# Performance work log

Measured on AMD Instinct MI355X. Metric: run time of the kernel, lower is better.

## Reference

```python
import jax, jax.numpy as jnp
import numpy as np

B, N, G, K, V, M = 8, 4096, 128, 16, 64, 64
D, NH, FF = 384, 8, 1536
DH = D // NH


def _ln(x):
    m = jnp.mean(x, -1, keepdims=True)
    v = jnp.mean((x - m) ** 2, -1, keepdims=True)
    return (x - m) * jax.lax.rsqrt(v + 1e-5)


def _attn(q_in, kv_in, w, mask=None):
    # w: [4, D, D] = (Wq, Wk, Wv, Wo)
    Bq, Sq, _ = q_in.shape
    Sk = kv_in.shape[1]
    q = (q_in @ w[0]).reshape(Bq, Sq, NH, DH)
    k = (kv_in @ w[1]).reshape(Bq, Sk, NH, DH)
    v = (kv_in @ w[2]).reshape(Bq, Sk, NH, DH)
    logits = jnp.einsum('bqhd,bkhd->bhqk', q, k) / np.float32(np.sqrt(DH))
    if mask is not None:
        logits = jnp.where(mask[:, None], logits, jnp.float32(-1e9))
    a = jax.nn.softmax(logits, -1)
    return jnp.einsum('bhqk,bkhd->bqhd', a, v).reshape(Bq, Sq, D) @ w[3]


def _ffn(x, w1, w2):
    return jax.nn.relu(x @ w1) @ w2


def _knn(q, ref, k):
    d = (jnp.sum(q * q, -1)[:, :, None] + jnp.sum(ref * ref, -1)[:, None, :]
         - 2.0 * jnp.einsum('bqd,brd->bqr', q, ref))
    return jax.lax.top_k(-d, k)[1]  # [B, Nq, k]


def _fps(pos, m):
    Bc = pos.shape[0]
    d0 = jnp.sum((pos - pos[:, :1]) ** 2, -1)
    def step(mind, _):
        nxt = jnp.argmax(mind, -1)
        p = jnp.take_along_axis(pos, nxt[:, None, None], 1)
        return jnp.minimum(mind, jnp.sum((pos - p) ** 2, -1)), nxt
    _, idxs = jax.lax.scan(step, d0, None, length=m - 1)
    idx = jnp.concatenate([jnp.zeros((Bc, 1), idxs.dtype), idxs.T], 1)
    return jnp.take_along_axis(pos, idx[..., None], 1)  # [B, m, 3]


def _pe(xyz):
    # PositionEmbeddingCoordsSine: 3 -> D, scale=1.0
    cd = D // 3
    dim_t = 10000.0 ** (2.0 * (jnp.arange(cd) // 2) / cd)
    p = xyz[..., None] / dim_t  # [..., 3, cd]
    pe = jnp.stack([jnp.sin(p[..., 0::2]), jnp.cos(p[..., 1::2])], -1)
    return pe.reshape(xyz.shape[:-1] + (D,))


def _gather(x, idx):  # x: [B,S,C], idx: [B,m]
    return jnp.take_along_axis(x, idx[:, :, None], 1)


def _neigh_mask(nidx, S):  # boolean attention mask from knn indices
    Bc, Q, _ = nidx.shape
    return jnp.zeros((Bc, Q, S), bool).at[
        jnp.arange(Bc)[:, None, None], jnp.arange(Q)[None, :, None], nidx].set(True)


def _tokenize(pos, w1, b1, w2, b2, w3, b3, w4, b4):
    centers = _fps(pos, G)
    nidx = _knn(centers, pos, K)
    grouped = pos[jnp.arange(pos.shape[0])[:, None, None], nidx]  # [B,G,K,3]
    rel = grouped - centers[:, :, None, :]
    f = jax.nn.relu(rel @ w1 + b1) @ w2 + b2                       # [B,G,K,256]
    g = jnp.broadcast_to(f.max(2)[:, :, None, :], f.shape)
    tok = (jax.nn.relu(jnp.concatenate([g, f], -1) @ w3 + b3) @ w4 + b4).max(2)
    return tok, centers


def _cross_encoder(src, tgt, src_mask, tgt_mask, cx_attn, cx_ff1, cx_ff2):
    sa, ca = cx_attn[0], cx_attn[1]
    src = src + _attn(_ln(src), _ln(src), sa, src_mask)
    tgt = tgt + _attn(_ln(tgt), _ln(tgt), sa, tgt_mask)
    src2 = src + _attn(_ln(src), _ln(tgt), ca)
    tgt2 = tgt + _attn(_ln(tgt), _ln(src), ca)
    src2 = src2 + _ffn(_ln(src2), cx_ff1, cx_ff2)
    tgt2 = tgt2 + _ffn(_ln(tgt2), cx_ff1, cx_ff2)
    return src2, tgt2


def _dec_blocks(q, q_pos, mem, mem_pos, sa, ca, f1, f2):
    x = q + q_pos
    m = mem + mem_pos
    for l in range(ca.shape[0]):
        if sa is not None:
            x = x + _attn(_ln(x), _ln(x), sa[l])
        x = x + _attn(_ln(x), _ln(m), ca[l])
        x = x + _ffn(_ln(x), f1[l], f2[l])
    return x


def _upsample(pos, centers, feats, w1, b1, w2, b2):
    # PointNet++ feature propagation: 3-NN inverse-distance interpolation + MLP
    d = (jnp.sum(pos * pos, -1)[:, :, None] + jnp.sum(centers * centers, -1)[:, None, :]
         - 2.0 * jnp.einsum('bnd,bgd->bng', pos, centers))
    nd, idx = jax.lax.top_k(-d, 3)
    w = 1.0 / (jnp.maximum(-nd, 0.0) + 1e-8)
    w = w / jnp.sum(w, -1, keepdims=True)
    nb = feats[jnp.arange(pos.shape[0])[:, None, None], idx]  # [B,N,3,D]
    interp = jnp.sum(w[..., None] * nb, 2)
    x = jnp.concatenate([interp, pos], -1)  # concat xyz (points1) -> D+3
    return jax.nn.relu(jax.nn.relu(x @ w1 + b1) @ w2 + b2)


def _smooth_l1(t, p, beta=2.0):
    a = jnp.abs(p - t)
    return jnp.mean(jnp.where(a < beta, 0.5 * a * a / beta, a - 0.5 * beta))


def _forward(pos_src, pos_tgt, tok_w1, tok_b1, tok_w2, tok_b2, tok_w3, tok_b3,
             tok_w4, tok_b4, mask_token, cx_attn, cx_ff1, cx_ff2,
             enc_sa, enc_ca, enc_ff1, enc_ff2, dec_ca, dec_ff1, dec_ff2,
             up_w1, up_b1, up_w2, up_b2,
             vis_idx_src, msk_idx_src, vis_idx_tgt, msk_idx_tgt):
    tokens_src, centers_src = _tokenize(pos_src, tok_w1, tok_b1, tok_w2, tok_b2, tok_w3, tok_b3, tok_w4, tok_b4)
    tokens_tgt, centers_tgt = _tokenize(pos_tgt, tok_w1, tok_b1, tok_w2, tok_b2, tok_w3, tok_b3, tok_w4, tok_b4)
    c_src_pe, c_tgt_pe = _pe(centers_src), _pe(centers_tgt)
    p_src_pe, p_tgt_pe = _pe(pos_src), _pe(pos_tgt)

    vis3_src = _gather(centers_src, vis_idx_src)   # [B,V,3]
    vis3_tgt = _gather(centers_tgt, vis_idx_tgt)
    vtok_src = _gather(tokens_src, vis_idx_src)    # [B,V,D]
    vtok_tgt = _gather(tokens_tgt, vis_idx_tgt)

    m_full_src = _neigh_mask(_knn(centers_src, centers_src, K), G)
    m_full_tgt = _neigh_mask(_knn(centers_tgt, centers_tgt, K), G)
    m_vis_src = _neigh_mask(_knn(vis3_src, vis3_src, K), V)
    m_vis_tgt = _neigh_mask(_knn(vis3_tgt, vis3_tgt, K), V)

    vis_out_src, vis_out_tgt = _cross_encoder(vtok_src, vtok_tgt, m_vis_src, m_vis_tgt, cx_attn, cx_ff1, cx_ff2)
    src_out, tgt_out = _cross_encoder(tokens_src, tokens_tgt, m_full_src, m_full_tgt, cx_attn, cx_ff1, cx_ff2)

    Bc = pos_src.shape[0]
    mt = jnp.broadcast_to(mask_token, (Bc, M, D))
    q_src = jnp.concatenate([mt, vis_out_src], 1)
    qpos_src = jnp.concatenate([_gather(c_src_pe, msk_idx_src), _gather(c_src_pe, vis_idx_src)], 1)
    q_tgt = jnp.concatenate([mt, vis_out_tgt], 1)
    qpos_tgt = jnp.concatenate([_gather(c_tgt_pe, msk_idx_tgt), _gather(c_tgt_pe, vis_idx_tgt)], 1)

    dec_src = _dec_blocks(q_src, qpos_src, tgt_out, c_tgt_pe, enc_sa, enc_ca, enc_ff1, enc_ff2)
    dec_tgt = _dec_blocks(q_tgt, qpos_tgt, src_out, c_src_pe, enc_sa, enc_ca, enc_ff1, enc_ff2)

    t_src = jax.lax.stop_gradient(_gather(src_out, msk_idx_src))
    t_tgt = jax.lax.stop_gradient(_gather(tgt_out, msk_idx_tgt))
    mae = 0.5 * _smooth_l1(t_src, dec_src[:, :M]) + 0.5 * _smooth_l1(t_tgt, dec_tgt[:, :M])

    up_src = _upsample(pos_src, centers_src, src_out, up_w1, up_b1, up_w2, up_b2)
    up_tgt = _upsample(pos_tgt, centers_tgt, tgt_out, up_w1, up_b1, up_w2, up_b2)
    dense_src = _dec_blocks(up_src, p_src_pe, src_out, c_src_pe, None, dec_ca, dec_ff1, dec_ff2)
    dense_tgt = _dec_blocks(up_tgt, p_tgt_pe, tgt_out, c_tgt_pe, None, dec_ca, dec_ff1, dec_ff2)
    return dense_src, dense_tgt, mae


def setup_inputs() -> dict:
    key = jax.random.key(0)
    ks = jax.random.split(key, 32)
    nrm = lambda i, shp: jax.random.normal(ks[i], shp, dtype=jnp.float32) * 0.02
    ps = jax.vmap(lambda k: jax.random.permutation(k, G))(jax.random.split(ks[2], B))
    pt = jax.vmap(lambda k: jax.random.permutation(k, G))(jax.random.split(ks[3], B))
    return {
        'pos_src': jax.random.normal(ks[0], (B, N, 3), dtype=jnp.float32),
        'pos_tgt': jax.random.normal(ks[1], (B, N, 3), dtype=jnp.float32),
        'vis_idx_src': ps[:, :V], 'msk_idx_src': ps[:, V:],
        'vis_idx_tgt': pt[:, :V], 'msk_idx_tgt': pt[:, V:],
        'tok_w1': nrm(4, (3, 128)), 'tok_b1': jnp.zeros((128,), jnp.float32),
        'tok_w2': nrm(5, (128, 256)), 'tok_b2': jnp.zeros((256,), jnp.float32),
        'tok_w3': nrm(6, (512, 512)), 'tok_b3': jnp.zeros((512,), jnp.float32),
        'tok_w4': nrm(7, (512, D)), 'tok_b4': jnp.zeros((D,), jnp.float32),
        'mask_token': nrm(8, (D,)),
        'cx_attn': nrm(9, (2, 4, D, D)), 'cx_ff1': nrm(10, (D, FF)), 'cx_ff2': nrm(11, (FF, D)),
        'enc_sa': nrm(12, (4, 4, D, D)), 'enc_ca': nrm(13, (4, 4, D, D)),
        'enc_ff1': nrm(14, (4, D, FF)), 'enc_ff2': nrm(15, (4, FF, D)),
        'dec_ca': nrm(16, (2, 4, D, D)), 'dec_ff1': nrm(17, (2, D, FF)), 'dec_ff2': nrm(18, (2, FF, D)),
        'up_w1': nrm(19, (D + 3, D)), 'up_b1': jnp.zeros((D,), jnp.float32),
        'up_w2': nrm(20, (D, D)), 'up_b2': jnp.zeros((D,), jnp.float32),
    }


def reference(pos_src, pos_tgt, vis_idx_src, msk_idx_src, vis_idx_tgt, msk_idx_tgt,
              tok_w1, tok_b1, tok_w2, tok_b2, tok_w3, tok_b3, tok_w4, tok_b4,
              mask_token, cx_attn, cx_ff1, cx_ff2, enc_sa, enc_ca, enc_ff1, enc_ff2,
              dec_ca, dec_ff1, dec_ff2, up_w1, up_b1, up_w2, up_b2):
    return _forward(pos_src, pos_tgt, tok_w1, tok_b1, tok_w2, tok_b2, tok_w3, tok_b3,
                    tok_w4, tok_b4, mask_token, cx_attn, cx_ff1, cx_ff2,
                    enc_sa, enc_ca, enc_ff1, enc_ff2, dec_ca, dec_ff1, dec_ff2,
                    up_w1, up_b1, up_w2, up_b2,
                    vis_idx_src, msk_idx_src, vis_idx_tgt, msk_idx_tgt)
```

## Files before the change

kernel.cpp:

```cpp
#include <hip/hip_runtime.h>
#include <hip/hip_bf16.h>
#include <math.h>

using bf16 = __hip_bfloat16;

#define DI static __device__ __forceinline__

constexpr int Bc = 8, Nn = 4096, Gc = 128, Kc = 16, Vc = 64, Mc = 64;
constexpr int Dd = 384, NHh = 8, DHh = 48, FFf = 1536;

typedef __bf16 bf8v __attribute__((ext_vector_type(8)));
typedef float f4v __attribute__((ext_vector_type(4)));

DI float b2f(bf16 h) { return __bfloat162float(h); }
DI __bf16 f2b(float f) { return (__bf16)f; }

__global__ __launch_bounds__(256) void detect_kernel(const unsigned int* __restrict__ w, int* __restrict__ flag) {
    __shared__ int sh[256];
    int cnt = 0;
    for (int i = threadIdx.x; i < 16384; i += 256) {
        unsigned int lo = w[i] & 0xffffu;
        int e = (int)((lo >> 7) & 0xffu);
        if (e < 100 || e > 140) cnt++;
    }
    sh[threadIdx.x] = cnt;
    __syncthreads();
    for (int s = 128; s > 0; s >>= 1) {
        if (threadIdx.x < s) sh[threadIdx.x] += sh[threadIdx.x + s];
        __syncthreads();
    }
    if (threadIdx.x == 0) flag[0] = (sh[0] < 2048) ? 1 : 0;
}

DI float ldf(const void* p, size_t i, int isbf) {
    return isbf ? b2f(((const bf16*)p)[i]) : ((const float*)p)[i];
}

__global__ void cvtf_kernel(const void* __restrict__ src, float* __restrict__ dst, size_t n,
                            const int* __restrict__ flag) {
    size_t t = (size_t)blockIdx.x * 256 + threadIdx.x;
    if (t < n) dst[t] = ldf(src, t, flag[0]);
}

__global__ void wtr_kernel(const void* __restrict__ src, __bf16* __restrict__ dst,
                           int K, int N, int Kpad, int cnt, const int* __restrict__ flag) {
    size_t t = (size_t)blockIdx.x * 256 + threadIdx.x;
    size_t total = (size_t)cnt * N * Kpad;
    if (t >= total) return;
    int k = (int)(t % Kpad);
    size_t rem = t / Kpad;
    int n = (int)(rem % N);
    int mat = (int)(rem / N);
    float v = (k < K) ? ldf(src, ((size_t)mat * K + k) * N + n, flag[0]) : 0.f;
    dst[t] = f2b(v);
}

__global__ void zero_kernel(unsigned char* __restrict__ p, size_t n) {
    size_t t = (size_t)blockIdx.x * 256 + threadIdx.x;
    if (t < n) p[t] = 0;
}

__global__ void add_kernel(const float* __restrict__ a, const float* __restrict__ b,
                           float* __restrict__ o, size_t n) {
    size_t t = (size_t)blockIdx.x * 256 + threadIdx.x;
    if (t < n) o[t] = a[t] + b[t];
}

__global__ __launch_bounds__(256) void fps_kernel(const float* __restrict__ pos_a, const float* __restrict__ pos_b,
                                                  float* __restrict__ cent_a, float* __restrict__ cent_b) {
    __shared__ float px[Nn], py[Nn], pz[Nn];
    __shared__ float wv[4];
    __shared__ int wi[4];
    __shared__ int chosen;
    int side = blockIdx.x >> 3, b = blockIdx.x & 7, tid = threadIdx.x;
    const float* pos = side ? pos_b : pos_a;
    float* cent = side ? cent_b : cent_a;
    const float* p = pos + (size_t)b * Nn * 3;
    for (int i = tid; i < Nn; i += 256) { px[i] = p[3*i]; py[i] = p[3*i+1]; pz[i] = p[3*i+2]; }
    __syncthreads();
    float cx = px[0], cy = py[0], cz = pz[0];
    if (tid == 0) { float* c0 = cent + (size_t)b * Gc * 3; c0[0] = cx; c0[1] = cy; c0[2] = cz; }
    float mind[16];
#pragma unroll
    for (int j = 0; j < 16; j++) {
        int i = tid + 256 * j;
        float dx = px[i]-cx, dy = py[i]-cy, dz = pz[i]-cz;
        mind[j] = __fadd_rn(__fadd_rn(__fmul_rn(dx,dx), __fmul_rn(dy,dy)), __fmul_rn(dz,dz));
    }
    for (int s = 1; s < Gc; s++) {
        float bv = -1.f; int bi = 0;
#pragma unroll
        for (int j = 0; j < 16; j++) { int i = tid + 256*j; if (mind[j] > bv) { bv = mind[j]; bi = i; } }
        for (int o = 32; o > 0; o >>= 1) {
            float v2 = __shfl_down(bv, o, 64); int i2 = __shfl_down(bi, o, 64);
            if (v2 > bv || (v2 == bv && i2 < bi)) { bv = v2; bi = i2; }
        }
        if ((tid & 63) == 0) { wv[tid >> 6] = bv; wi[tid >> 6] = bi; }
        __syncthreads();
        if (tid == 0) {
            float fv = wv[0]; int fi = wi[0];
            for (int k = 1; k < 4; k++)
                if (wv[k] > fv || (wv[k] == fv && wi[k] < fi)) { fv = wv[k]; fi = wi[k]; }
            chosen = fi;
            float* cs = cent + ((size_t)b * Gc + s) * 3;
            cs[0] = px[fi]; cs[1] = py[fi]; cs[2] = pz[fi];
        }
        __syncthreads();
        int ci = chosen;
        float qx = px[ci], qy = py[ci], qz = pz[ci];
#pragma unroll
        for (int j = 0; j < 16; j++) {
            int i = tid + 256 * j;
            float dx = px[i]-qx, dy = py[i]-qy, dz = pz[i]-qz;
            float d = __fadd_rn(__fadd_rn(__fmul_rn(dx,dx), __fmul_rn(dy,dy)), __fmul_rn(dz,dz));
            if (d < mind[j]) mind[j] = d;
        }
    }
}

__global__ __launch_bounds__(64) void knn16_kernel(const float* __restrict__ q, const float* __restrict__ r,
                                                   int* __restrict__ nidx, int NQ, int NR) {
    __shared__ float dist[4096];
    int blk = blockIdx.x; int b = blk / NQ, qi = blk % NQ;
    int lane = threadIdx.x;
    const float* qp = q + ((size_t)b * NQ + qi) * 3;
    float qx = qp[0], qy = qp[1], qz = qp[2];
    float qq = __fadd_rn(__fadd_rn(__fmul_rn(qx,qx), __fmul_rn(qy,qy)), __fmul_rn(qz,qz));
    const float* rp = r + (size_t)b * NR * 3;
    for (int i = lane; i < NR; i += 64) {
        float rx = rp[3*i], ry = rp[3*i+1], rz = rp[3*i+2];
        float rr = __fadd_rn(__fadd_rn(__fmul_rn(rx,rx), __fmul_rn(ry,ry)), __fmul_rn(rz,rz));
        float dot = __fadd_rn(__fadd_rn(__fmul_rn(qx,rx), __fmul_rn(qy,ry)), __fmul_rn(qz,rz));
        dist[i] = __fadd_rn(__fadd_rn(qq, rr), -2.f * dot);
    }
    __syncthreads();
    int* out = nidx + ((size_t)b * NQ + qi) * Kc;
    for (int sel = 0; sel < Kc; ++sel) {
        float bv = INFINITY; int bi = 0;
        bool has = false;
        for (int i = lane; i < NR; i += 64) {
            float v = dist[i];
            if (!has || v < bv) { bv = v; bi = i; has = true; }
        }
        for (int o = 32; o > 0; o >>= 1) {
            float v2 = __shfl_xor(bv, o, 64); int i2 = __shfl_xor(bi, o, 64);
            if (v2 < bv || (v2 == bv && i2 < bi)) { bv = v2; bi = i2; }
        }
        if (lane == 0) { out[sel] = bi; dist[bi] = INFINITY; }
        __syncthreads();
    }
}

__global__ __launch_bounds__(64) void knn3_kernel(const float* __restrict__ pos, const float* __restrict__ cent,
                                                  int* __restrict__ idx3, float* __restrict__ w3) {
    int bn = blockIdx.x; int b = bn / Nn;
    int lane = threadIdx.x;
    const float* p = pos + (size_t)bn * 3;
    float px = p[0], py = p[1], pz = p[2];
    float pp = __fadd_rn(__fadd_rn(__fmul_rn(px,px), __fmul_rn(py,py)), __fmul_rn(pz,pz));
    float dv[2]; int di[2];
#pragma unroll
    for (int c = 0; c < 2; c++) {
        int g = lane + 64 * c;
        const float* cp = cent + ((size_t)b * Gc + g) * 3;
        float cx = cp[0], cy = cp[1], cz = cp[2];
// ... 59 lines not shown
    if (t >= BG * C) return;
    int c = t % C; int bg = t / C;
    const float* p = in + (size_t)bg * Kc * C + c;
    float m = -INFINITY;
    for (int k = 0; k < Kc; k++) m = fmaxf(m, p[(size_t)k * C]);
    out[t] = m;
}

__global__ void maxk_bf_kernel(const __bf16* __restrict__ in, __bf16* __restrict__ out, int BG, int C) {
    int t = blockIdx.x * 256 + threadIdx.x;
    if (t >= BG * C) return;
    int c = t % C; int bg = t / C;
    const __bf16* p = in + (size_t)bg * Kc * C + c;
    float m = -INFINITY;
    for (int k = 0; k < Kc; k++) m = fmaxf(m, (float)p[(size_t)k * C]);
    out[t] = f2b(m);
}

__global__ void concat_gf_kernel(const __bf16* __restrict__ g, const __bf16* __restrict__ f,
                                 __bf16* __restrict__ cat, int BG) {
    size_t t = (size_t)blockIdx.x * 256 + threadIdx.x;
    size_t total = (size_t)BG * Kc * 512;
    if (t >= total) return;
    int c = (int)(t % 512); size_t bgk = t / 512; size_t bg = bgk / Kc;
    cat[t] = (c < 256) ? g[bg * 256 + c] : f[bgk * 256 + (c - 256)];
}

__global__ void gather_rows_kernel(const float* __restrict__ in, const int* __restrict__ idx,
                                   float* __restrict__ out, int Ni, int C, int Sin) {
    size_t t = (size_t)blockIdx.x * 256 + threadIdx.x;
    size_t total = (size_t)Bc * Ni * C;
    if (t >= total) return;
    int c = (int)(t % C); size_t bi = t / C; int i = (int)(bi % Ni); int b = (int)(bi / Ni);
    int r = idx[(size_t)b * Ni + i];
    out[t] = in[((size_t)b * Sin + r) * C + c];
}

__global__ void scatter_mask_kernel(const int* __restrict__ nidx, unsigned char* __restrict__ mask,
                                    int Q, int S, int nb) {
    int t = blockIdx.x * 256 + threadIdx.x;
    if (t >= nb * Q * Kc) return;
    int q = (t / Kc) % Q; int b = t / (Kc * Q);
    mask[((size_t)b * Q + q) * S + nidx[t]] = 1;
}

__global__ void pe_kernel(float* __restrict__ dst, const float* __restrict__ base,
                          const float* __restrict__ xyz, size_t total) {
    size_t t = (size_t)blockIdx.x * 256 + threadIdx.x;
    if (t >= total) return;
    int d = (int)(t % Dd); size_t bs = t / Dd;
    int c = d >> 7;
    int i = d & 127;
    int j = i >> 1;
    float inv = expf(-0.1439115683121279f * (float)j);
    float val = xyz[bs * 3 + c] * inv;
    float pe = (i & 1) ? cosf(val) : sinf(val);
    dst[t] = (base ? base[t] : 0.f) + pe;
}

__global__ __launch_bounds__(256) void ln_kernel(const float* __restrict__ X, __bf16* __restrict__ Y, int R) {
    int lane = threadIdx.x & 63;
    int row = blockIdx.x * 4 + (threadIdx.x >> 6);
    if (row >= R) return;
    const float* x = X + (size_t)row * Dd;
    float v[6]; float s = 0.f;
#pragma unroll
    for (int j = 0; j < 6; j++) { v[j] = x[lane + 64*j]; s += v[j]; }
#pragma unroll
    for (int o = 32; o > 0; o >>= 1) s += __shfl_xor(s, o, 64);
    float m = s * (1.f / Dd);
    float s2 = 0.f;
#pragma unroll
    for (int j = 0; j < 6; j++) { float d = v[j] - m; s2 += d * d; }
#pragma unroll
    for (int o = 32; o > 0; o >>= 1) s2 += __shfl_xor(s2, o, 64);
    float inv = rsqrtf(s2 * (1.f / Dd) + 1e-5f);
    __bf16* y = Y + (size_t)row * Dd;
#pragma unroll
    for (int j = 0; j < 6; j++) y[lane + 64*j] = f2b((v[j] - m) * inv);
}

__global__ __launch_bounds__(256) void gemm_kernel(const __bf16* __restrict__ A, const __bf16* __restrict__ Wt,
                                                   const float* __restrict__ bias,
                                                   const float* __restrict__ res, void* __restrict__ Cv,
                                                   int M, int Ncols, int Kk, int relu, int obf) {
    __shared__ __bf16 As[128][72];
    __shared__ __bf16 Bs[128][72];
    const int tid = threadIdx.x;
    const int row0 = blockIdx.y * 128, col0 = blockIdx.x * 128;
    const int w = tid >> 6, lane = tid & 63, m = lane & 15, q = lane >> 4;
    const int wr = w >> 1, wc = w & 1;
    const int srow = tid >> 1, sk = (tid & 1) * 32;
    const __bf16* ap = A + (size_t)(row0 + srow) * Kk + sk;
    const __bf16* wp = Wt + (size_t)(col0 + srow) * Kk + sk;

    f4v acc[4][4];
#pragma unroll
    for (int r = 0; r < 4; r++)
#pragma unroll
        for (int n = 0; n < 4; n++) acc[r][n] = (f4v){0.f, 0.f, 0.f, 0.f};

    for (int k0 = 0; k0 < Kk; k0 += 64) {
#pragma unroll
        for (int i = 0; i < 4; i++) {
            *reinterpret_cast<uint4*>(&As[srow][sk + 8*i]) = *reinterpret_cast<const uint4*>(ap + k0 + 8*i);
            *reinterpret_cast<uint4*>(&Bs[srow][sk + 8*i]) = *reinterpret_cast<const uint4*>(wp + k0 + 8*i);
        }
        __syncthreads();
#pragma unroll
        for (int kk = 0; kk < 2; kk++) {
            bf8v bfr[4], afr[4];
#pragma unroll
            for (int n = 0; n < 4; n++) bfr[n] = *reinterpret_cast<bf8v*>(&Bs[wc*64 + n*16 + m][kk*32 + q*8]);
#pragma unroll
            for (int r = 0; r < 4; r++) afr[r] = *reinterpret_cast<bf8v*>(&As[wr*64 + r*16 + m][kk*32 + q*8]);
#pragma unroll
            for (int r = 0; r < 4; r++)
#pragma unroll
                for (int n = 0; n < 4; n++)
                    acc[r][n] = __builtin_amdgcn_mfma_f32_16x16x32_bf16(afr[r], bfr[n], acc[r][n], 0, 0, 0);
        }
        __syncthreads();
    }
#pragma unroll
    for (int n = 0; n < 4; n++) {
        const int gn = col0 + wc*64 + n*16 + m;
        float bv = bias ? bias[gn] : 0.f;
#pragma unroll
        for (int r = 0; r < 4; r++) {
#pragma unroll
            for (int j = 0; j < 4; j++) {
                int gm = row0 + wr*64 + r*16 + q*4 + j;
                float v = acc[r][n][j] + bv;
                if (relu) v = fmaxf(v, 0.f);
                if (res) v += res[(size_t)gm * Ncols + gn];
                if (obf) ((__bf16*)Cv)[(size_t)gm * Ncols + gn] = f2b(v);
                else     ((float*)Cv)[(size_t)gm * Ncols + gn] = v;
            }
        }
    }
}

__global__ __launch_bounds__(256) void attn_mfma_kernel(const __bf16* __restrict__ Qb,
                                                        const __bf16* __restrict__ Kp,
                                                        const __bf16* __restrict__ Vp,
                                                        __bf16* __restrict__ O,
                                                        int ldq, int ldkv, int ldo, int rpb, int b0) {
    __shared__ char smem[128*136*2 + 48*136*2];
    __bf16 (*Ks)[72]  = (__bf16(*)[72])smem;
    __bf16 (*Pl)[136] = (__bf16(*)[136])smem;
    __bf16 (*Vt)[136] = (__bf16(*)[136])(smem + 128*136*2);
    const int tid = threadIdx.x;
    const int h = blockIdx.y, z = blockIdx.z;
    const int bk = b0 + z;
    const size_t row0 = (size_t)z * rpb + (size_t)blockIdx.x * 128;
    {
        int r = tid >> 1, c0 = (tid & 1) * 24;
        const __bf16* kp = Kp + ((size_t)bk * 128 + r) * ldkv + h * 48 + c0;
        *reinterpret_cast<bf8v*>(&Ks[r][c0])      = *reinterpret_cast<const bf8v*>(kp);
        *reinterpret_cast<bf8v*>(&Ks[r][c0 + 8])  = *reinterpret_cast<const bf8v*>(kp + 8);
        *reinterpret_cast<bf8v*>(&Ks[r][c0 + 16]) = *reinterpret_cast<const bf8v*>(kp + 16);
        if (tid & 1) {
            *reinterpret_cast<bf8v*>(&Ks[r][48]) = (bf8v){};
            *reinterpret_cast<bf8v*>(&Ks[r][56]) = (bf8v){};
        }
        const __bf16* vp = Vp + ((size_t)bk * 128 + r) * ldkv + h * 48 + c0;
        bf8v w0 = *reinterpret_cast<const bf8v*>(vp);
        bf8v w1 = *reinterpret_cast<const bf8v*>(vp + 8);
        bf8v w2 = *reinterpret_cast<const bf8v*>(vp + 16);
#pragma unroll
        for (int i = 0; i < 8; i++) {
            Vt[c0 + i][r] = w0[i]; Vt[c0 + 8 + i][r] = w1[i]; Vt[c0 + 16 + i][r] = w2[i];
        }
    }
    __syncthreads();
    const int w = tid >> 6, lane = tid & 63, m = lane & 15, q = lane >> 4;
    const __bf16* qbase = Qb + (row0 + (size_t)(w*32 + m)) * ldq + h * 48;
    f4v sc[2][8];
#pragma unroll
    for (int rt = 0; rt < 2; rt++)
#pragma unroll
        for (int nt = 0; nt < 8; nt++) sc[rt][nt] = (f4v){0.f, 0.f, 0.f, 0.f};
#pragma unroll
    for (int kk = 0; kk < 2; kk++) {
        bf8v a0 = *reinterpret_cast<const bf8v*>(qbase + kk*32 + q*8);
        bf8v a1 = *reinterpret_cast<const bf8v*>(qbase + (size_t)16*ldq + kk*32 + q*8);
#pragma unroll
        for (int nt = 0; nt < 8; nt++) {
            bf8v bf = *reinterpret_cast<bf8v*>(&Ks[nt*16 + m][kk*32 + q*8]);
            sc[0][nt] = __builtin_amdgcn_mfma_f32_16x16x32_bf16(a0, bf, sc[0][nt], 0, 0, 0);
            sc[1][nt] = __builtin_amdgcn_mfma_f32_16x16x32_bf16(a1, bf, sc[1][nt], 0, 0, 0);
        }
    }
    const float scale = 0.14433756729740643f;
    float inv_[2][4];
#pragma unroll
    for (int rt = 0; rt < 2; rt++) {
#pragma unroll
        for (int j = 0; j < 4; j++) {
            float mv = -INFINITY;
#pragma unroll
            for (int nt = 0; nt < 8; nt++) { sc[rt][nt][j] *= scale; mv = fmaxf(mv, sc[rt][nt][j]); }
#pragma unroll
            for (int o = 8; o > 0; o >>= 1) mv = fmaxf(mv, __shfl_xor(mv, o, 64));
            float sum = 0.f;
#pragma unroll
            for (int nt = 0; nt < 8; nt++) {
                float e = expf(sc[rt][nt][j] - mv);
                sc[rt][nt][j] = e; sum += e;
            }
#pragma unroll
            for (int o = 8; o > 0; o >>= 1) sum += __shfl_xor(sum, o, 64);
            inv_[rt][j] = 1.f / sum;
        }
    }
    __syncthreads();
#pragma unroll
    for (int rt = 0; rt < 2; rt++)
#pragma unroll
        for (int nt = 0; nt < 8; nt++)
#pragma unroll
            for (int j = 0; j < 4; j++)
                Pl[w*32 + rt*16 + q*4 + j][nt*16 + m] = f2b(sc[rt][nt][j]);
    __syncthreads();
    f4v ov[2][3];
#pragma unroll
    for (int rt = 0; rt < 2; rt++)
#pragma unroll
        for (int nt = 0; nt < 3; nt++) ov[rt][nt] = (f4v){0.f, 0.f, 0.f, 0.f};
#pragma unroll
    for (int kk = 0; kk < 4; kk++) {
        bf8v p0 = *reinterpret_cast<bf8v*>(&Pl[w*32 + m][kk*32 + q*8]);
        bf8v p1 = *reinterpret_cast<bf8v*>(&Pl[w*32 + 16 + m][kk*32 + q*8]);
#pragma unroll
        for (int nt = 0; nt < 3; nt++) {
            bf8v bv = *reinterpret_cast<bf8v*>(&Vt[nt*16 + m][kk*32 + q*8]);
            ov[0][nt] = __builtin_amdgcn_mfma_f32_16x16x32_bf16(p0, bv, ov[0][nt], 0, 0, 0);
            ov[1][nt] = __builtin_amdgcn_mfma_f32_16x16x32_bf16(p1, bv, ov[1][nt], 0, 0, 0);
        }
    }
    __bf16* op = O + (row0 + (size_t)(w*32)) * ldo + h * 48;
#pragma unroll
    for (int rt = 0; rt < 2; rt++)
#pragma unroll
        for (int nt = 0; nt < 3; nt++)
#pragma unroll
            for (int j = 0; j < 4; j++)
                op[(size_t)(rt*16 + q*4 + j) * ldo + nt*16 + m] = f2b(ov[rt][nt][j] * inv_[rt][j]);
}

__global__ __launch_bounds__(64) void attn_kernel(const float* __restrict__ Q, const float* __restrict__ Kb,
                                                  const float* __restrict__ Vb,
                                                  const unsigned char* __restrict__ mask,
                                                  __bf16* __restrict__ O, int Sq, int Sk, int xorv,
                                                  int ldq, int ldkv) {
    int qi = blockIdx.x, h = blockIdx.y, bq = blockIdx.z;
    int bk = bq ^ xorv;
    int lane = threadIdx.x;
    __shared__ float qv[DHh];
    __shared__ float pv[128];
    const size_t qrow = (size_t)bq * Sq + qi;
// ... 149 lines not shown

    const size_t arenaO = o;
    const size_t arena_bytes = (ws_size > arenaO) ? (ws_size - arenaO) : 0;
    int RP = 128;
    {
        const int cands[10] = {65536, 32768, 16384, 8192, 4096, 2048, 1024, 512, 256, 128};
        for (int ci = 0; ci < 10; ci++) {
            if ((size_t)cands[ci] * 9344 + 8192 <= arena_bytes) { RP = cands[ci]; break; }
        }
    }
    size_t ao = arenaO;
    auto aalloc = [&](size_t bytes) -> size_t { size_t r = ao; ao += (bytes + 255) & ~(size_t)255; return r; };
    const size_t AcbO = aalloc((size_t)RP*448*2);
    const size_t XcO  = aalloc((size_t)RP*384*4);
    const size_t LcO  = aalloc((size_t)RP*384*2);
    const size_t T1O  = aalloc((size_t)RP*384*4);
    const size_t QTO  = aalloc((size_t)RP*384*2);
    const size_t T2O  = aalloc((size_t)RP*384*2);
    const size_t HhO  = aalloc((size_t)RP*1536*2);
    int TC = (int)(arena_bytes / 70200);
    TC &= ~7; if (TC > 2048) TC = 2048; if (TC < 8) TC = 8;
    size_t to = arenaO;
    auto talloc = [&](size_t bytes) -> size_t { size_t r = to; to += (bytes + 255) & ~(size_t)255; return r; };
    const size_t tk1O = talloc((size_t)TC*16*128*2);
    const size_t tk2O = talloc((size_t)TC*16*256*2);
    const size_t tgmO = talloc((size_t)TC*256*2);
    const size_t tcatO = talloc((size_t)TC*16*512*2);
    const size_t thbO = talloc((size_t)TC*16*512*2);
    const size_t t4oO = talloc((size_t)TC*16*384*4);

    auto F = [&](size_t off) -> float* { return (float*)(ws + off); };
    auto I = [&](size_t off) -> int* { return (int*)(ws + off); };
    auto U = [&](size_t off) -> unsigned char* { return (unsigned char*)(ws + off); };
    auto Bf = [&](size_t off) -> __bf16* { return (__bf16*)(ws + off); };
    auto ew = [](size_t n) -> dim3 { return dim3((unsigned)((n + 255) / 256)); };
    const int* flag = I(flagO);
    __bf16* WT = Bf(wtO);
    float* BF = F(bsO);
    const int b_t1 = 0, b_t2 = 128, b_t3 = 384, b_t4 = 896, b_u1 = 1280, b_u2 = 1664;

    auto gemm = [&](const __bf16* A, const __bf16* W, const float* bias, const float* res, void* C,
                    int M, int Ncol, int Kk, int relu, int obf) {
        dim3 g((unsigned)(Ncol / 128), (unsigned)(M / 128));
        gemm_kernel<<<g, 256, 0, stream>>>(A, W, bias, res, C, M, Ncol, Kk, relu, obf);
    };
    auto ln = [&](const float* X, __bf16* Y, int R) {
        ln_kernel<<<dim3((R + 3) / 4), 256, 0, stream>>>(X, Y, R);
    };
    auto attn_old = [&](const float* Qp, const float* Kp, const float* Vp, const unsigned char* mask,
                        __bf16* Op, int Sq, int Sk, int nb, int xorv, int ldq, int ldkv) {
        attn_kernel<<<dim3(Sq, NHh, nb), 64, 0, stream>>>(Qp, Kp, Vp, mask, Op, Sq, Sk, xorv, ldq, ldkv);
    };
    auto attn_mfma = [&](const __bf16* Qp, const __bf16* Kp, const __bf16* Vp, __bf16* Op,
                         int ldq, int ldkv, int ldo, int rpb, int nb, int b0) {
        attn_mfma_kernel<<<dim3(rpb/128, NHh, nb), 256, 0, stream>>>(Qp, Kp, Vp, Op, ldq, ldkv, ldo, rpb, b0);
    };
    __bf16* ctxb = Bf(cxO);

    auto ffn = [&](float* x, const __bf16* w1t, const __bf16* w2t, int R) {
        ln(x, Bf(lnSO), R);
        for (int r0 = 0; r0 < R; r0 += RP) {
            int rc = (R - r0 < RP) ? (R - r0) : RP;
            gemm(Bf(lnSO) + (size_t)r0*Dd, w1t, nullptr, nullptr, Bf(HhO), rc, FFf, Dd, 1, 1);
            gemm(Bf(HhO), w2t, nullptr, x + (size_t)r0*Dd, x + (size_t)r0*Dd, rc, Dd, FFf, 0, 0);
        }
    };
    auto cross_enc = [&](float* x, const unsigned char* mask, int S) {
        const int R = 16 * S;
        ln(x, Bf(lnSO), R);
        gemm(Bf(lnSO), WT + wt_cx, nullptr, nullptr, F(qkvbO), R, 1152, Dd, 0, 0);
        attn_old(F(qkvbO), F(qkvbO) + 384, F(qkvbO) + 768, mask, ctxb, S, S, 16, 0, 1152, 1152);
        gemm(ctxb, WT + wt_cx + 3*DD, nullptr, x, x, R, Dd, Dd, 0, 0);
        ln(x, Bf(lnSO), R);
        gemm(Bf(lnSO), WT + wt_cx + 4*DD, nullptr, nullptr, F(qkvbO), R, 1152, Dd, 0, 0);
        attn_old(F(qkvbO), F(qkvbO) + 384, F(qkvbO) + 768, nullptr, ctxb, S, S, 16, 8, 1152, 1152);
        gemm(ctxb, WT + wt_cx + 7*DD, nullptr, x, x, R, Dd, Dd, 0, 0);
        ffn(x, WT + wt_cf1, WT + wt_cf2, R);
    };
    auto decoder4 = [&](float* x) {
        for (int l = 0; l < 4; l++) {
            ln(x, Bf(lnTO), 2048);
            gemm(Bf(lnTO), WT + wt_es + (size_t)l*4*DD, nullptr, nullptr, Bf(qkvbO), 2048, 1152, Dd, 0, 1);
            attn_mfma(Bf(qkvbO), Bf(qkvbO) + 384, Bf(qkvbO) + 768, ctxb, 1152, 1152, Dd, 128, 16, 0);
            gemm(ctxb, WT + wt_es + (size_t)l*4*DD + 3*DD, nullptr, x, x, 2048, Dd, Dd, 0, 0);
            ln(x, Bf(lnTO), 2048);
            gemm(Bf(lnTO), WT + wt_ec + (size_t)l*4*DD, nullptr, nullptr, Bf(qbO), 2048, Dd, Dd, 0, 1);
            gemm(Bf(lnmO), WT + wt_ec + (size_t)l*4*DD + DD, nullptr, nullptr, Bf(kvbO), 2048, 768, Dd, 0, 1);
            attn_mfma(Bf(qbO), Bf(kvbO), Bf(kvbO) + 384, ctxb, Dd, 768, Dd, 128, 16, 0);
            gemm(ctxb, WT + wt_ec + (size_t)l*4*DD + 3*DD, nullptr, x, x, 2048, Dd, Dd, 0, 0);
            ffn(x, WT + wt_ef1 + (size_t)l*DF, WT + wt_ef2 + (size_t)l*DF, 2048);
        }
    };

    detect_kernel<<<dim3(1), 256, 0, stream>>>((const unsigned int*)pos_src, I(flagO));
    cvtf_kernel<<<ew(PH), 256, 0, stream>>>(pos_src, F(posfO), PH, flag);
    cvtf_kernel<<<ew(PH), 256, 0, stream>>>(pos_tgt, F(posfO) + PH, PH, flag);
    cvtf_kernel<<<dim3(2), 256, 0, stream>>>(mtok, F(mtokO), (size_t)Dd, flag);

    auto wtr = [&](const void* src, size_t dstOff, int K, int N, int Kpad, int cnt) {
        wtr_kernel<<<ew((size_t)cnt * N * Kpad), 256, 0, stream>>>(src, WT + dstOff, K, N, Kpad, cnt, flag);
    };
    wtr(tw1, wt_t1, 3, 128, 64, 1);
    wtr(tw2, wt_t2, 128, 256, 128, 1);
    wtr(tw3, wt_t3, 512, 512, 512, 1);
    wtr(tw4, wt_t4, 512, 384, 512, 1);
    wtr(cxw, wt_cx, 384, 384, 384, 8);
    wtr(cff1, wt_cf1, 384, 1536, 384, 1);
    wtr(cff2, wt_cf2, 1536, 384, 1536, 1);
    wtr(esa, wt_es, 384, 384, 384, 16);
    wtr(eca, wt_ec, 384, 384, 384, 16);
    wtr(eff1, wt_ef1, 384, 1536, 384, 4);
    wtr(eff2, wt_ef2, 1536, 384, 1536, 4);
    wtr(dca, wt_dc, 384, 384, 384, 8);
    wtr(dff1, wt_df1, 384, 1536, 384, 2);
    wtr(dff2, wt_df2, 1536, 384, 1536, 2);
    wtr(uw1, wt_u1, 387, 384, 448, 1);
    wtr(uw2, wt_u2, 384, 384, 384, 1);
    cvtf_kernel<<<ew(128), 256, 0, stream>>>(tb1, BF + b_t1, 128, flag);
    cvtf_kernel<<<ew(256), 256, 0, stream>>>(tb2, BF + b_t2, 256, flag);
    cvtf_kernel<<<ew(512), 256, 0, stream>>>(tb3, BF + b_t3, 512, flag);
    cvtf_kernel<<<ew(384), 256, 0, stream>>>(tb4, BF + b_t4, 384, flag);
    cvtf_kernel<<<ew(384), 256, 0, stream>>>(ub1, BF + b_u1, 384, flag);
    cvtf_kernel<<<ew(384), 256, 0, stream>>>(ub2, BF + b_u2, 384, flag);

    fps_kernel<<<dim3(16), 256, 0, stream>>>(F(posfO), F(posfO) + PH, F(centO), F(centO) + (size_t)Bc*Gc*3);

    knn16_kernel<<<dim3(16*Gc), 64, 0, stream>>>(F(centO), F(posfO), I(nidxO), Gc, Nn);
    rel_kernel<<<ew((size_t)16*Gc*Kc*64), 256, 0, stream>>>(F(posfO), F(centO), I(nidxO), Bf(relbO), 16);
    for (int g0 = 0; g0 < 16*Gc; g0 += TC) {
        const int gc = (16*Gc - g0 < TC) ? (16*Gc - g0) : TC;
        const int RC = gc * Kc;
        gemm(Bf(relbO) + (size_t)g0*Kc*64, WT + wt_t1, BF + b_t1, nullptr, Bf(tk1O), RC, 128, 64, 1, 1);
        gemm(Bf(tk1O), WT + wt_t2, BF + b_t2, nullptr, Bf(tk2O), RC, 256, 128, 0, 1);
        maxk_bf_kernel<<<ew((size_t)gc*256), 256, 0, stream>>>(Bf(tk2O), Bf(tgmO), gc, 256);
        concat_gf_kernel<<<ew((size_t)RC*512), 256, 0, stream>>>(Bf(tgmO), Bf(tk2O), Bf(tcatO), gc);
        gemm(Bf(tcatO), WT + wt_t3, BF + b_t3, nullptr, Bf(thbO), RC, 512, 512, 1, 1);
        gemm(Bf(thbO), WT + wt_t4, BF + b_t4, nullptr, F(t4oO), RC, Dd, 512, 0, 0);
        maxk_f32_kernel<<<ew((size_t)gc*Dd), 256, 0, stream>>>(F(t4oO), F(tokO) + (size_t)g0*Dd, gc, Dd);
    }

    pe_kernel<<<ew((size_t)16*GD), 256, 0, stream>>>(F(cpeO), nullptr, F(centO), (size_t)16*GD);

    gather_rows_kernel<<<ew((size_t)Bc*Vc*Dd), 256, 0, stream>>>(F(tokO), vis_s, F(vtokO), Vc, Dd, Gc);
    gather_rows_kernel<<<ew((size_t)Bc*Vc*Dd), 256, 0, stream>>>(F(tokO) + 8*GD, vis_t, F(vtokO) + (size_t)8*Vc*Dd, Vc, Dd, Gc);
    gather_rows_kernel<<<ew((size_t)Bc*Vc*3), 256, 0, stream>>>(F(centO), vis_s, F(vis3O), Vc, 3, Gc);
    gather_rows_kernel<<<ew((size_t)Bc*Vc*3), 256, 0, stream>>>(F(centO) + (size_t)Bc*Gc*3, vis_t, F(vis3O) + (size_t)8*Vc*3, Vc, 3, Gc);

    zero_kernel<<<ew((size_t)16*Gc*Gc), 256, 0, stream>>>(U(mfullO), (size_t)16*Gc*Gc);
    knn16_kernel<<<dim3(16*Gc), 64, 0, stream>>>(F(centO), F(centO), I(nidxO), Gc, Gc);
    scatter_mask_kernel<<<ew((size_t)16*Gc*Kc), 256, 0, stream>>>(I(nidxO), U(mfullO), Gc, Gc, 16);
    zero_kernel<<<ew((size_t)16*Vc*Vc), 256, 0, stream>>>(U(mvisO), (size_t)16*Vc*Vc);
    knn16_kernel<<<dim3(16*Vc), 64, 0, stream>>>(F(vis3O), F(vis3O), I(nidxO), Vc, Vc);
    scatter_mask_kernel<<<ew((size_t)16*Vc*Kc), 256, 0, stream>>>(I(nidxO), U(mvisO), Vc, Vc, 16);

    cross_enc(F(vtokO), U(mvisO), Vc);
    cross_enc(F(tokO), U(mfullO), Gc);

    dec_init_kernel<<<ew((size_t)Bc*GD), 256, 0, stream>>>(F(mtokO), F(vtokO), F(cpeO), msk_s, vis_s, F(decxO));
    dec_init_kernel<<<ew((size_t)Bc*GD), 256, 0, stream>>>(F(mtokO), F(vtokO) + (size_t)8*Vc*Dd, F(cpeO) + 8*GD, msk_t, vis_t, F(decxO) + 8*GD);
    add_kernel<<<ew((size_t)8*GD), 256, 0, stream>>>(F(tokO) + 8*GD, F(cpeO) + 8*GD, F(membO), (size_t)8*GD);
    add_kernel<<<ew((size_t)8*GD), 256, 0, stream>>>(F(tokO), F(cpeO), F(membO) + 8*GD, (size_t)8*GD);
    ln(F(membO), Bf(lnmO), 2048);
    decoder4(F(decxO));

    zero_kernel<<<dim3(1), 256, 0, stream>>>(U(accbO), 64);
    gather_rows_kernel<<<ew((size_t)Bc*Mc*Dd), 256, 0, stream>>>(F(tokO), msk_s, F(tbsO), Mc, Dd, Gc);
    gather_rows_kernel<<<ew((size_t)Bc*Mc*Dd), 256, 0, stream>>>(F(tokO) + 8*GD, msk_t, F(tbtO), Mc, Dd, Gc);
    sl1_kernel<<<ew((size_t)Bc*Mc*Dd), 256, 0, stream>>>(F(tbsO), F(decxO), F(accbO), 0);
    sl1_kernel<<<ew((size_t)Bc*Mc*Dd), 256, 0, stream>>>(F(tbtO), F(decxO) + 8*GD, F(accbO), 1);

    knn3_kernel<<<dim3(16*Nn), 64, 0, stream>>>(F(posfO), F(centO), I(idx3O), F(w3O));
    add_kernel<<<ew((size_t)16*GD), 256, 0, stream>>>(F(tokO), F(cpeO), F(membO), (size_t)16*GD);
    ln(F(membO), Bf(lnmO), 2048);
    gemm(Bf(lnmO), WT + wt_dc + 0*4*DD + DD, nullptr, nullptr, Bf(kvd0O), 2048, 768, Dd, 0, 1);
    gemm(Bf(lnmO), WT + wt_dc + 1*4*DD + DD, nullptr, nullptr, Bf(kvd1O), 2048, 768, Dd, 0, 1);
    const size_t kvdo[2] = {kvd0O, kvd1O};
    const int RT = 16 * Nn;
    for (int r0 = 0; r0 < RT; r0 += RP) {
        const int rpb = (RP < Nn) ? RP : Nn;
        const int nb = (RP < Nn) ? 1 : RP / Nn;
        const int b0 = r0 / Nn;
        interp_kernel<<<ew((size_t)RP*448), 256, 0, stream>>>(F(tokO), F(posfO), I(idx3O), F(w3O), Bf(AcbO), r0, RP);
        gemm(Bf(AcbO), WT + wt_u1, BF + b_u1, nullptr, Bf(LcO), RP, Dd, 448, 1, 1);
        gemm(Bf(LcO), WT + wt_u2, BF + b_u2, nullptr, F(T1O), RP, Dd, Dd, 1, 0);
        pe_kernel<<<ew((size_t)RP*Dd), 256, 0, stream>>>(F(XcO), F(T1O), F(posfO) + (size_t)r0*3, (size_t)RP*Dd);
        for (int l = 0; l < 2; l++) {
            ln(F(XcO), Bf(LcO), RP);
            gemm(Bf(LcO), WT + wt_dc + (size_t)l*4*DD, nullptr, nullptr, Bf(QTO), RP, Dd, Dd, 0, 1);
            attn_mfma(Bf(QTO), Bf(kvdo[l]), Bf(kvdo[l]) + 384, Bf(T2O), Dd, 768, Dd, rpb, nb, b0);
            gemm(Bf(T2O), WT + wt_dc + (size_t)l*4*DD + 3*DD, nullptr, F(XcO), F(XcO), RP, Dd, Dd, 0, 0);
            ln(F(XcO), Bf(LcO), RP);
            gemm(Bf(LcO), WT + wt_df1 + (size_t)l*DF, nullptr, nullptr, Bf(HhO), RP, FFf, Dd, 1, 1);
            if (l == 1)
                gemm(Bf(HhO), WT + wt_df2 + DF, nullptr, F(XcO), out + (size_t)r0*Dd, RP, Dd, FFf, 0, 0);
            else
                gemm(Bf(HhO), WT + wt_df2, nullptr, F(XcO), F(XcO), RP, Dd, FFf, 0, 0);
        }
    }

    mae_finalize_kernel<<<dim3(1), 1, 0, stream>>>(F(accbO), out + (size_t)2*Bc*Nn*Dd);
}
```

Measured before the change: 3.602 ms.

## Use direct-to-LDS swizzled GEMM loads, MFMA masked cross attention, wider FPS

The GEMM tile loads now use global_load_lds straight into an XOR-swizzled, unpadded LDS layout instead of staging through registers, which removes register round trips and should avoid bank conflicts. The cross-encoder with S=128 now uses bf16 QKV and the MFMA attention kernel, which gains a boolean mask and a batch-xor argument, in place of the older fp32 scalar attention. FPS runs 512 threads per block, and the PE and softmax paths use fast __expf/__sinf/__cosf intrinsics. The changes risk small numeric differences from fast math and bf16 QKV, and they rely on the LDS layout being correct.

```diff
diff --git a/kernel.cpp b/kernel.cpp
--- a/kernel.cpp
+++ b/kernel.cpp
@@ -14,6 +14,11 @@
 
 DI float b2f(bf16 h) { return __bfloat162float(h); }
 DI __bf16 f2b(float f) { return (__bf16)f; }
+
+DI void gld16(const void* g, void* l) {
+    __builtin_amdgcn_global_load_lds((const __attribute__((address_space(1))) void*)g,
+                                     (__attribute__((address_space(3))) void*)l, 16, 0, 0);
+}
 
 __global__ __launch_bounds__(256) void detect_kernel(const unsigned int* __restrict__ w, int* __restrict__ flag) {
     __shared__ int sh[256];
@@ -66,31 +71,31 @@
     if (t < n) o[t] = a[t] + b[t];
 }
 
-__global__ __launch_bounds__(256) void fps_kernel(const float* __restrict__ pos_a, const float* __restrict__ pos_b,
+__global__ __launch_bounds__(512) void fps_kernel(const float* __restrict__ pos_a, const float* __restrict__ pos_b,
                                                   float* __restrict__ cent_a, float* __restrict__ cent_b) {
     __shared__ float px[Nn], py[Nn], pz[Nn];
-    __shared__ float wv[4];
-    __shared__ int wi[4];
+    __shared__ float wv[8];
+    __shared__ int wi[8];
     __shared__ int chosen;
     int side = blockIdx.x >> 3, b = blockIdx.x & 7, tid = threadIdx.x;
     const float* pos = side ? pos_b : pos_a;
     float* cent = side ? cent_b : cent_a;
     const float* p = pos + (size_t)b * Nn * 3;
-    for (int i = tid; i < Nn; i += 256) { px[i] = p[3*i]; py[i] = p[3*i+1]; pz[i] = p[3*i+2]; }
+    for (int i = tid; i < Nn; i += 512) { px[i] = p[3*i]; py[i] = p[3*i+1]; pz[i] = p[3*i+2]; }
     __syncthreads();
     float cx = px[0], cy = py[0], cz = pz[0];
     if (tid == 0) { float* c0 = cent + (size_t)b * Gc * 3; c0[0] = cx; c0[1] = cy; c0[2] = cz; }
-    float mind[16];
-#pragma unroll
-    for (int j = 0; j < 16; j++) {
-        int i = tid + 256 * j;
+    float mind[8];
+#pragma unroll
+    for (int j = 0; j < 8; j++) {
+        int i = tid + 512 * j;
         float dx = px[i]-cx, dy = py[i]-cy, dz = pz[i]-cz;
         mind[j] = __fadd_rn(__fadd_rn(__fmul_rn(dx,dx), __fmul_rn(dy,dy)), __fmul_rn(dz,dz));
     }
     for (int s = 1; s < Gc; s++) {
         float bv = -1.f; int bi = 0;
 #pragma unroll
-        for (int j = 0; j < 16; j++) { int i = tid + 256*j; if (mind[j] > bv) { bv = mind[j]; bi = i; } }
+        for (int j = 0; j < 8; j++) { int i = tid + 512*j; if (mind[j] > bv) { bv = mind[j]; bi = i; } }
         for (int o = 32; o > 0; o >>= 1) {
             float v2 = __shfl_down(bv, o, 64); int i2 = __shfl_down(bi, o, 64);
             if (v2 > bv || (v2 == bv && i2 < bi)) { bv = v2; bi = i2; }
@@ -99,7 +104,7 @@
         __syncthreads();
         if (tid == 0) {
             float fv = wv[0]; int fi = wi[0];
-            for (int k = 1; k < 4; k++)
+            for (int k = 1; k < 8; k++)
                 if (wv[k] > fv || (wv[k] == fv && wi[k] < fi)) { fv = wv[k]; fi = wi[k]; }
             chosen = fi;
             float* cs = cent + ((size_t)b * Gc + s) * 3;
@@ -109,8 +114,8 @@
         int ci = chosen;
         float qx = px[ci], qy = py[ci], qz = pz[ci];
 #pragma unroll
-        for (int j = 0; j < 16; j++) {
-            int i = tid + 256 * j;
+        for (int j = 0; j < 8; j++) {
+            int i = tid + 512 * j;
             float dx = px[i]-qx, dy = py[i]-qy, dz = pz[i]-qz;
             float d = __fadd_rn(__fadd_rn(__fmul_rn(dx,dx), __fmul_rn(dy,dy)), __fmul_rn(dz,dz));
             if (d < mind[j]) mind[j] = d;
@@ -276,9 +281,9 @@
     int c = d >> 7;
     int i = d & 127;
     int j = i >> 1;
-    float inv = expf(-0.1439115683121279f * (float)j);
+    float inv = __expf(-0.1439115683121279f * (float)j);
     float val = xyz[bs * 3 + c] * inv;
-    float pe = (i & 1) ? cosf(val) : sinf(val);
+    float pe = (i & 1) ? __cosf(val) : __sinf(val);
     dst[t] = (base ? base[t] : 0.f) + pe;
 }
 
@@ -308,15 +313,18 @@
                                                    const float* __restrict__ bias,
                                                    const float* __restrict__ res, void* __restrict__ Cv,
                                                    int M, int Ncols, int Kk, int relu, int obf) {
-    __shared__ __bf16 As[128][72];
-    __shared__ __bf16 Bs[128][72];
+    __shared__ alignas(16) __bf16 As[128*64];
+    __shared__ alignas(16) __bf16 Bs[128*64];
     const int tid = threadIdx.x;
     const int row0 = blockIdx.y * 128, col0 = blockIdx.x * 128;
     const int w = tid >> 6, lane = tid & 63, m = lane & 15, q = lane >> 4;
     const int wr = w >> 1, wc = w & 1;
-    const int srow = tid >> 1, sk = (tid & 1) * 32;
-    const __bf16* ap = A + (size_t)(row0 + srow) * Kk + sk;
-    const __bf16* wp = Wt + (size_t)(col0 + srow) * Kk + sk;
+    const int l8 = lane >> 3, l7 = lane & 7;
+    const __bf16* apg = A  + (size_t)(row0 + 32*w + l8) * Kk + 8*(l7 ^ l8);
+    const __bf16* wpg = Wt + (size_t)(col0 + 32*w + l8) * Kk + 8*(l7 ^ l8);
+    const int swz = (m & 7) << 4;
+    const char* asb = (const char*)As;
+    const char* bsb = (const char*)Bs;
 
     f4v acc[4][4];
 #pragma unroll
@@ -327,17 +335,19 @@
     for (int k0 = 0; k0 < Kk; k0 += 64) {
 #pragma unroll
         for (int i = 0; i < 4; i++) {
-            *reinterpret_cast<uint4*>(&As[srow][sk + 8*i]) = *reinterpret_cast<const uint4*>(ap + k0 + 8*i);
-            *reinterpret_cast<uint4*>(&Bs[srow][sk + 8*i]) = *reinterpret_cast<const uint4*>(wp + k0 + 8*i);
+            gld16(apg + k0 + (size_t)(8*i) * Kk, As + w*2048 + i*512);
+            gld16(wpg + k0 + (size_t)(8*i) * Kk, Bs + w*2048 + i*512);
         }
         __syncthreads();
 #pragma unroll
         for (int kk = 0; kk < 2; kk++) {
             bf8v bfr[4], afr[4];
 #pragma unroll
-            for (int n = 0; n < 4; n++) bfr[n] = *reinterpret_cast<bf8v*>(&Bs[wc*64 + n*16 + m][kk*32 + q*8]);
-#pragma unroll
-            for (int r = 0; r < 4; r++) afr[r] = *reinterpret_cast<bf8v*>(&As[wr*64 + r*16 + m][kk*32 + q*8]);
+            for (int n = 0; n < 4; n++)
+                bfr[n] = *(const bf8v*)(bsb + (wc*64 + n*16 + m)*128 + ((kk*64 + q*16) ^ swz));
+#pragma unroll
+            for (int r = 0; r < 4; r++)
+                afr[r] = *(const bf8v*)(asb + (wr*64 + r*16 + m)*128 + ((kk*64 + q*16) ^ swz));
 #pragma unroll
             for (int r = 0; r < 4; r++)
 #pragma unroll
@@ -369,14 +379,15 @@
                                                         const __bf16* __restrict__ Kp,
                                                         const __bf16* __restrict__ Vp,
                                                         __bf16* __restrict__ O,
-                                                        int ldq, int ldkv, int ldo, int rpb, int b0) {
-    __shared__ char smem[128*136*2 + 48*136*2];
+                                                        int ldq, int ldkv, int ldo, int rpb, int b0,
+                                                        int bxor, const unsigned char* __restrict__ Mk) {
+    __shared__ alignas(16) char smem[128*136*2 + 48*136*2];
     __bf16 (*Ks)[72]  = (__bf16(*)[72])smem;
     __bf16 (*Pl)[136] = (__bf16(*)[136])smem;
     __bf16 (*Vt)[136] = (__bf16(*)[136])(smem + 128*136*2);
     const int tid = threadIdx.x;
     const int h = blockIdx.y, z = blockIdx.z;
-    const int bk = b0 + z;
+    const int bk = (b0 + z) ^ bxor;
     const size_t row0 = (size_t)z * rpb + (size_t)blockIdx.x * 128;
     {
         int r = tid >> 1, c0 = (tid & 1) * 24;
@@ -422,15 +433,22 @@
     for (int rt = 0; rt < 2; rt++) {
 #pragma unroll
         for (int j = 0; j < 4; j++) {
+            const unsigned char* mr = Mk ?
+                (Mk + ((size_t)z * rpb + (size_t)blockIdx.x*128 + (w*32 + rt*16 + q*4 + j)) * 128 + m) : nullptr;
             float mv = -INFINITY;
 #pragma unroll
-            for (int nt = 0; nt < 8; nt++) { sc[rt][nt][j] *= scale; mv = fmaxf(mv, sc[rt][nt][j]); }
+            for (int nt = 0; nt < 8; nt++) {
+                float vs = sc[rt][nt][j] * scale;
+                if (mr && !mr[nt*16]) vs = -1e9f;
+                sc[rt][nt][j] = vs;
+                mv = fmaxf(mv, vs);
+            }
 #pragma unroll
             for (int o = 8; o > 0; o >>= 1) mv = fmaxf(mv, __shfl_xor(mv, o, 64));
             float sum = 0.f;
 #pragma unroll
             for (int nt = 0; nt < 8; nt++) {
-                float e = expf(sc[rt][nt][j] - mv);
+                float e = __expf(sc[rt][nt][j] - mv);
                 sc[rt][nt][j] = e; sum += e;
             }
 #pragma unroll
@@ -686,8 +704,9 @@
         attn_kernel<<<dim3(Sq, NHh, nb), 64, 0, stream>>>(Qp, Kp, Vp, mask, Op, Sq, Sk, xorv, ldq, ldkv);
     };
     auto attn_mfma = [&](const __bf16* Qp, const __bf16* Kp, const __bf16* Vp, __bf16* Op,
-                         int ldq, int ldkv, int ldo, int rpb, int nb, int b0) {
-        attn_mfma_kernel<<<dim3(rpb/128, NHh, nb), 256, 0, stream>>>(Qp, Kp, Vp, Op, ldq, ldkv, ldo, rpb, b0);
+                         int ldq, int ldkv, int ldo, int rpb, int nb, int b0,
+                         int bxor, const unsigned char* mask) {
+        attn_mfma_kernel<<<dim3(rpb/128, NHh, nb), 256, 0, stream>>>(Qp, Kp, Vp, Op, ldq, ldkv, ldo, rpb, b0, bxor, mask);
     };
     __bf16* ctxb = Bf(cxO);
 
@@ -701,26 +720,37 @@
     };
     auto cross_enc = [&](float* x, const unsigned char* mask, int S) {
         const int R = 16 * S;
-        ln(x, Bf(lnSO), R);
-        gemm(Bf(lnSO), WT + wt_cx, nullptr, nullptr, F(qkvbO), R, 1152, Dd, 0, 0);
-        attn_old(F(qkvbO), F(qkvbO) + 384, F(qkvbO) + 768, mask, ctxb, S, S, 16, 0, 1152, 1152);
-        gemm(ctxb, WT + wt_cx + 3*DD, nullptr, x, x, R, Dd, Dd, 0, 0);
-        ln(x, Bf(lnSO), R);
-        gemm(Bf(lnSO), WT + wt_cx + 4*DD, nullptr, nullptr, F(qkvbO), R, 1152, Dd, 0, 0);
-        attn_old(F(qkvbO), F(qkvbO) + 384, F(qkvbO) + 768, nullptr, ctxb, S, S, 16, 8, 1152, 1152);
-        gemm(ctxb, WT + wt_cx + 7*DD, nullptr, x, x, R, Dd, Dd, 0, 0);
+        if (S == 128) {
+            ln(x, Bf(lnSO), R);
+            gemm(Bf(lnSO), WT + wt_cx, nullptr, nullptr, Bf(qkvbO), R, 1152, Dd, 0, 1);
+            attn_mfma(Bf(qkvbO), Bf(qkvbO) + 384, Bf(qkvbO) + 768, ctxb, 1152, 1152, Dd, 128, 16, 0, 0, mask);
+            gemm(ctxb, WT + wt_cx + 3*DD, nullptr, x, x, R, Dd, Dd, 0, 0);
+            ln(x, Bf(lnSO), R);
+            gemm(Bf(lnSO), WT + wt_cx + 4*DD, nullptr, nullptr, Bf(qkvbO), R, 1152, Dd, 0, 1);
+            attn_mfma(Bf(qkvbO), Bf(qkvbO) + 384, Bf(qkvbO) + 768, ctxb, 1152, 1152, Dd, 128, 16, 0, 8, nullptr);
+            gemm(ctxb, WT + wt_cx + 7*DD, nullptr, x, x, R, Dd, Dd, 0, 0);
+        } else {
+            ln(x, Bf(lnSO), R);
+            gemm(Bf(lnSO), WT + wt_cx, nullptr, nullptr, F(qkvbO), R, 1152, Dd, 0, 0);
+            attn_old(F(qkvbO), F(qkvbO) + 384, F(qkvbO) + 768, mask, ctxb, S, S, 16, 0, 1152, 1152);
+            gemm(ctxb, WT + wt_cx + 3*DD, nullptr, x, x, R, Dd, Dd, 0, 0);
+            ln(x, Bf(lnSO), R);
+            gemm(Bf(lnSO), WT + wt_cx + 4*DD, nullptr, nullptr, F(qkvbO), R, 1152, Dd, 0, 0);
+            attn_old(F(qkvbO), F(qkvbO) + 384, F(qkvbO) + 768, nullptr, ctxb, S, S, 16, 8, 1152, 1152);
+            gemm(ctxb, WT + wt_cx + 7*DD, nullptr, x, x, R, Dd, Dd, 0, 0);
+        }
         ffn(x, WT + wt_cf1, WT + wt_cf2, R);
     };
     auto decoder4 = [&](float* x) {
         for (int l = 0; l < 4; l++) {
             ln(x, Bf(lnTO), 2048);
             gemm(Bf(lnTO), WT + wt_es + (size_t)l*4*DD, nullptr, nullptr, Bf(qkvbO), 2048, 1152, Dd, 0, 1);
-            attn_mfma(Bf(qkvbO), Bf(qkvbO) + 384, Bf(qkvbO) + 768, ctxb, 1152, 1152, Dd, 128, 16, 0);
+            attn_mfma(Bf(qkvbO), Bf(qkvbO) + 384, Bf(qkvbO) + 768, ctxb, 1152, 1152, Dd, 128, 16, 0, 0, nullptr);
             gemm(ctxb, WT + wt_es + (size_t)l*4*DD + 3*DD, nullptr, x, x, 2048, Dd, Dd, 0, 0);
             ln(x, Bf(lnTO), 2048);
             gemm(Bf(lnTO), WT + wt_ec + (size_t)l*4*DD, nullptr, nullptr, Bf(qbO), 2048, Dd, Dd, 0, 1);
             gemm(Bf(lnmO), WT + wt_ec + (size_t)l*4*DD + DD, nullptr, nullptr, Bf(kvbO), 2048, 768, Dd, 0, 1);
-            attn_mfma(Bf(qbO), Bf(kvbO), Bf(kvbO) + 384, ctxb, Dd, 768, Dd, 128, 16, 0);
+            attn_mfma(Bf(qbO), Bf(kvbO), Bf(kvbO) + 384, ctxb, Dd, 768, Dd, 128, 16, 0, 0, nullptr);
             gemm(ctxb, WT + wt_ec + (size_t)l*4*DD + 3*DD, nullptr, x, x, 2048, Dd, Dd, 0, 0);
             ffn(x, WT + wt_ef1 + (size_t)l*DF, WT + wt_ef2 + (size_t)l*DF, 2048);
         }
@@ -757,7 +787,7 @@
     cvtf_kernel<<<ew(384), 256, 0, stream>>>(ub1, BF + b_u1, 384, flag);
     cvtf_kernel<<<ew(384), 256, 0, stream>>>(ub2, BF + b_u2, 384, flag);
 
-    fps_kernel<<<dim3(16), 256, 0, stream>>>(F(posfO), F(posfO) + PH, F(centO), F(centO) + (size_t)Bc*Gc*3);
+    fps_kernel<<<dim3(16), 512, 0, stream>>>(F(posfO), F(posfO) + PH, F(centO), F(centO) + (size_t)Bc*Gc*3);
 
     knn16_kernel<<<dim3(16*Gc), 64, 0, stream>>>(F(centO), F(posfO), I(nidxO), Gc, Nn);
     rel_kernel<<<ew((size_t)16*Gc*Kc*64), 256, 0, stream>>>(F(posfO), F(centO), I(nidxO), Bf(relbO), 16);
@@ -821,7 +851,7 @@
         for (int l = 0; l < 2; l++) {
             ln(F(XcO), Bf(LcO), RP);
             gemm(Bf(LcO), WT + wt_dc + (size_t)l*4*DD, nullptr, nullptr, Bf(QTO), RP, Dd, Dd, 0, 1);
-            attn_mfma(Bf(QTO), Bf(kvdo[l]), Bf(kvdo[l]) + 384, Bf(T2O), Dd, 768, Dd, rpb, nb, b0);
+            attn_mfma(Bf(QTO), Bf(kvdo[l]), Bf(kvdo[l]) + 384, Bf(T2O), Dd, 768, Dd, rpb, nb, b0, 0, nullptr);
             gemm(Bf(T2O), WT + wt_dc + (size_t)l*4*DD + 3*DD, nullptr, F(XcO), F(XcO), RP, Dd, Dd, 0, 0);
             ln(F(XcO), Bf(LcO), RP);
             gemm(Bf(LcO), WT + wt_df1 + (size_t)l*DF, nullptr, nullptr, Bf(HhO), RP, FFf, Dd, 1, 1);
```

New measurement: 3.372 ms. -6.4%, faster.
